# Optimization experiments

Hardware: AMD Instinct MI355X
Metric: run time of the kernel (lower is better)

The kernel has to match this reference:

```python
import jax, jax.numpy as jnp
from jax import lax
import numpy as np

B, C, H, W = 8, 1024, 32, 32
M = 32768
EPS = 1e-12  # clamp before sqrt, matching typical torch euclidean_dist


def setup_inputs() -> dict:
    key = jax.random.key(0)
    k1, k2 = jax.random.split(key)
    features = jax.random.normal(k1, (B, C, H, W), dtype=jnp.float32)
    coreset = jax.random.normal(k2, (M, C), dtype=jnp.float32)
    return {"features": features, "coreset": coreset}


def reference(features, coreset):
    # F.avg_pool2d(features, 3, 1, 1): kernel 3, stride 1, pad 1,
    # count_include_pad=True (torch default) -> window sum / 9.
    pooled = lax.reduce_window(
        features, jnp.float32(0.0), lax.add,
        window_dimensions=(1, 1, 3, 3),
        window_strides=(1, 1, 1, 1),
        padding=((0, 0), (0, 0), (1, 1), (1, 1)),
    ) / jnp.float32(9.0)
    # permute(0,2,3,1).view(B, H*W, C) then flatten batch -> [N, C]
    emb = pooled.transpose(0, 2, 3, 1).reshape(-1, C)  # [N=B*H*W, C]
    x2 = jnp.sum(emb * emb, axis=-1, keepdims=True)        # [N, 1]
    y2 = jnp.sum(coreset * coreset, axis=-1)               # [M]
    d2 = x2 + y2[None, :] - 2.0 * (emb @ coreset.T)        # [N, M]
    dist = jnp.sqrt(jnp.clip(d2, EPS))
    min_dist = jnp.min(dist, axis=1)                       # [N] 1-NN distance
    return min_dist
```

## Files before the change

### kernel.cpp

```cpp
#include <hip/hip_runtime.h>
#include <stdint.h>
#include <math.h>


#define N_TOT 8192
#define M_TOT 32768
#define EPS_ 1e-12f

typedef short bf16x8 __attribute__((ext_vector_type(8)));
typedef float f32x4 __attribute__((ext_vector_type(4)));

__device__ __forceinline__ unsigned short f2bf_rne(float f) {
    unsigned u = __float_as_uint(f);
    u += 0x7fffu + ((u >> 16) & 1u);
    return (unsigned short)(u >> 16);
}
__device__ __forceinline__ float bf2f(unsigned short h) {
    return __uint_as_float(((unsigned)h) << 16);
}

__global__ void init_kernel(unsigned* __restrict__ d2u, float* __restrict__ x2) {
    int i = blockIdx.x * blockDim.x + threadIdx.x;
    if (i < N_TOT) { d2u[i] = 0x7F800000u; x2[i] = 0.0f; }
}

__global__ __launch_bounds__(256) void pool_kernel(const float* __restrict__ feat,
                                                   unsigned short* __restrict__ emb,
                                                   float* __restrict__ x2) {
    int bid = blockIdx.x;
    int h  = bid & 31;
    int cc = (bid >> 5) & 31;
    int b  = bid >> 10;
    int tid = threadIdx.x;
    __shared__ float lds[32 * 97];

    const float* base = feat + ((size_t)(b * 1024 + cc * 32)) * 1024;
    int g0 = (h - 1) * 32;
    #pragma unroll
    for (int it = 0; it < 12; ++it) {
        int e = tid + it * 256;
        int ci = e / 96;
        int j  = e - ci * 96;
        int g  = g0 + j;
        float v = 0.0f;
        if (g >= 0 && g < 1024) v = base[(size_t)ci * 1024 + g];
        lds[ci * 97 + j] = v;
    }
    __syncthreads();

    int c  = tid & 31;
    int wb = tid >> 5;
    const float inv9 = 1.0f / 9.0f;
    #pragma unroll
    for (int i = 0; i < 4; ++i) {
        int w = wb + i * 8;
        float s = 0.0f;
        #pragma unroll
        for (int rr = 0; rr < 3; ++rr) {
            int rb = c * 97 + rr * 32 + w;
            s += lds[rb];
            if (w > 0)  s += lds[rb - 1];
            if (w < 31) s += lds[rb + 1];
        }
        float p = s * inv9;
        unsigned short bh = f2bf_rne(p);
        int n = b * 1024 + h * 32 + w;
        emb[(size_t)n * 1024 + cc * 32 + c] = bh;
        float pf = bf2f(bh);
        float sq = pf * pf;
        #pragma unroll
        for (int off = 1; off < 32; off <<= 1) sq += __shfl_xor(sq, off);
        if (c == 0) atomicAdd(&x2[n], sq);
    }
}

__global__ __launch_bounds__(256) void cs_kernel(const float* __restrict__ cs,
                                                 unsigned short* __restrict__ csb,
                                                 float* __restrict__ y2) {
    int row  = blockIdx.x * 4 + (threadIdx.x >> 6);
    int lane = threadIdx.x & 63;
    const float4* src = reinterpret_cast<const float4*>(cs + (size_t)row * 1024);
    ushort4* dst = reinterpret_cast<ushort4*>(csb + (size_t)row * 1024);
    float s = 0.0f;
    #pragma unroll
    for (int it = 0; it < 4; ++it) {
        float4 v = src[lane + it * 64];
        ushort4 o;
        o.x = f2bf_rne(v.x); o.y = f2bf_rne(v.y);
        o.z = f2bf_rne(v.z); o.w = f2bf_rne(v.w);
        dst[lane + it * 64] = o;
        float a = bf2f(o.x), b = bf2f(o.y), c = bf2f(o.z), d = bf2f(o.w);
        s += a * a + b * b + c * c + d * d;
    }
    #pragma unroll
    for (int off = 1; off < 64; off <<= 1) s += __shfl_xor(s, off);
    if (lane == 0) y2[row] = s;
}


#define STAGE(BUF, TT) do {                                                              \
    int t_ = (TT);                                                                       \
    _Pragma("unroll")                                                                    \
    for (int s_ = 0; s_ < 2; ++s_) {                                                     \
        __builtin_amdgcn_global_load_lds(                                                \
            (const __attribute__((address_space(1))) void*)(gA + (size_t)(s_ * 128 + rowq) * 1024 + t_ * 32 + ch * 8), \
            (__attribute__((address_space(3))) void*)(&lds[(BUF) * 16384 + s_ * 4096 + tid * 8]), 16, 0, 0); \
        __builtin_amdgcn_global_load_lds(                                                \
            (const __attribute__((address_space(1))) void*)(gB + (size_t)(s_ * 128 + rowq) * 1024 + t_ * 32 + ch * 8), \
            (__attribute__((address_space(3))) void*)(&lds[(BUF) * 16384 + 8192 + s_ * 4096 + tid * 8]), 16, 0, 0); \
    }                                                                                    \
} while (0)

#define READS_MFMA(BCUR) do {                                                            \
    bf16x8 af[8], bv[4];                                                                 \
    const unsigned short* pA = &lds[(BCUR) * 16384 + (wmBase + fr) * 32 + sx];           \
    const unsigned short* pB = &lds[(BCUR) * 16384 + 8192 + (wnBase + fr) * 32 + sx];    \
    _Pragma("unroll")                                                                    \
    for (int m = 0; m < 8; ++m) af[m] = *reinterpret_cast<const bf16x8*>(pA + m * 512);  \
    _Pragma("unroll")                                                                    \
    for (int n = 0; n < 4; ++n) bv[n] = *reinterpret_cast<const bf16x8*>(pB + n * 512);  \
    __builtin_amdgcn_s_setprio(1);                                                       \
    _Pragma("unroll")                                                                    \
    for (int m = 0; m < 8; ++m)                                                          \
        _Pragma("unroll")                                                                \
        for (int n = 0; n < 4; ++n)                                                      \
            acc[m][n] = __builtin_amdgcn_mfma_f32_16x16x32_bf16(af[m], bv[n], acc[m][n], 0, 0, 0); \
    __builtin_amdgcn_s_setprio(0);                                                       \
} while (0)

#define GEMM_ITER(BCUR, BSTG, TN) do {                                                   \
    asm volatile("s_waitcnt vmcnt(4)" ::: "memory");                                     \
    __builtin_amdgcn_s_barrier();                                                        \
    __builtin_amdgcn_sched_barrier(0);                                                   \
    STAGE(BSTG, TN);                                                                     \
    READS_MFMA(BCUR);                                                                    \
} while (0)

__global__ __launch_bounds__(512, 2) void gemm_min_kernel(const unsigned short* __restrict__ emb,
                                                          const unsigned short* __restrict__ csb,
                                                          const float* __restrict__ x2,
                                                          const float* __restrict__ y2,
                                                          unsigned* __restrict__ d2u) {
    __shared__ unsigned short lds[49152];

    int bid = blockIdx.x;
    int xcd   = bid & 7;
    int local = bid >> 3;
    int st    = local >> 4;
    int idx   = local & 15;
    int si = idx >> 2, sj = idx & 3;
    int emb_tile = (st & 7) * 4 + si;
    int cs_tile  = xcd * 16 + (st >> 3) * 4 + sj;
    int nb = emb_tile * 256;
    int mb = cs_tile * 256;

    int tid  = threadIdx.x;
    int lane = tid & 63;
    int wid  = tid >> 6;
    int wmBase = (wid >> 2) * 128;
    int wnBase = (wid & 3) * 64;

    int rowq = tid >> 2;
    int ch   = (tid & 3) ^ ((tid >> 3) & 3);
    const unsigned short* gA = emb + (size_t)nb * 1024;
    const unsigned short* gB = csb + (size_t)mb * 1024;

    int fr = lane & 15;
    int kq = lane >> 4;
    int sx = (kq ^ ((fr >> 1) & 3)) * 8;

    f32x4 acc[8][4];
    #pragma unroll
    for (int m = 0; m < 8; ++m)
        #pragma unroll
        for (int n = 0; n < 4; ++n) acc[m][n] = (f32x4){0.f, 0.f, 0.f, 0.f};

    STAGE(0, 0);
    STAGE(1, 1);

    #pragma unroll 1
    for (int u = 0; u < 30; u += 3) {
        GEMM_ITER(0, 2, u + 2);
        GEMM_ITER(1, 0, u + 3);
        GEMM_ITER(2, 1, u + 4);
    }
    asm volatile("s_waitcnt vmcnt(4)" ::: "memory");
    __builtin_amdgcn_s_barrier();
    __builtin_amdgcn_sched_barrier(0);
    READS_MFMA(0);
    asm volatile("s_waitcnt vmcnt(0)" ::: "memory");
    __builtin_amdgcn_s_barrier();
    __builtin_amdgcn_sched_barrier(0);
    READS_MFMA(1);

    int cc = lane & 15;
    int rq = (lane >> 4) * 4;
    float y2v[4];
    #pragma unroll
    for (int n = 0; n < 4; ++n) y2v[n] = y2[mb + wnBase + n * 16 + cc];

    #pragma unroll
    for (int m = 0; m < 8; ++m) {
        #pragma unroll
        for (int j = 0; j < 4; ++j) {
            float v = y2v[0] - 2.0f * acc[m][0][j];
            #pragma unroll
            for (int n = 1; n < 4; ++n) v = fminf(v, y2v[n] - 2.0f * acc[m][n][j]);
            int grow = nb + wmBase + m * 16 + rq + j;
            float d2 = x2[grow] + v;
            d2 = fmaxf(d2, EPS_);
            #pragma unroll
            for (int off = 1; off < 16; off <<= 1) d2 = fminf(d2, __shfl_xor(d2, off));
            if (cc == 0) atomicMin(&d2u[grow], __float_as_uint(d2));
        }
    }
}

__global__ void sqrt_kernel(const unsigned* __restrict__ d2u, float* __restrict__ out) {
    int i = blockIdx.x * blockDim.x + threadIdx.x;
    if (i < N_TOT) out[i] = sqrtf(__uint_as_float(d2u[i]));
}

extern "C" void kernel_launch(void* const* d_in, const int* in_sizes, int n_in,
                              void* d_out, int out_size, void* d_ws, size_t ws_size,
                              hipStream_t stream) {
    const float* feat = (const float*)d_in[0];
    const float* cs   = (const float*)d_in[1];
    float* out = (float*)d_out;

    char* ws = (char*)d_ws;
    unsigned short* emb = (unsigned short*)ws;
    unsigned short* csb = (unsigned short*)(ws + 16777216);
    float* x2 = (float*)(ws + 16777216 + 67108864);
    float* y2 = x2 + N_TOT;
    unsigned* d2u = (unsigned*)(y2 + M_TOT);

    init_kernel<<<N_TOT / 256, 256, 0, stream>>>(d2u, x2);
    pool_kernel<<<8192, 256, 0, stream>>>(feat, emb, x2);
    cs_kernel<<<M_TOT / 4, 256, 0, stream>>>(cs, csb, y2);
    gemm_min_kernel<<<4096, 512, 0, stream>>>(emb, csb, x2, y2, d2u);
    sqrt_kernel<<<N_TOT / 256, 256, 0, stream>>>(d2u, out);
}
```

Measured before the change: 905.9 us.

## Split each K-step into four barrier-synced phases interleaving LDS reads, staging and MFMA

Measured after the change: 891.0 us. Within noise of the previous version (-1.6%).

```diff
diff --git a/kernel.cpp b/kernel.cpp
--- a/kernel.cpp
+++ b/kernel.cpp
@@ -111,29 +111,53 @@
     }                                                                                    \
 } while (0)
 
-#define READS_MFMA(BCUR) do {                                                            \
-    bf16x8 af[8], bv[4];                                                                 \
-    const unsigned short* pA = &lds[(BCUR) * 16384 + (wmBase + fr) * 32 + sx];           \
-    const unsigned short* pB = &lds[(BCUR) * 16384 + 8192 + (wnBase + fr) * 32 + sx];    \
+#define STAGE_ONE(BSTG, TT, MTX, HALF)                                                   \
+    __builtin_amdgcn_global_load_lds(                                                    \
+        (const __attribute__((address_space(1))) void*)(((MTX) ? gB : gA) + (size_t)((HALF) * 128 + rowq) * 1024 + (TT) * 32 + ch * 8), \
+        (__attribute__((address_space(3))) void*)(&lds[(BSTG) * 16384 + (MTX) * 8192 + (HALF) * 4096 + tid * 8]), 16, 0, 0)
+
+#define PHASE_CORE(Q, A0, A1) do {                                                       \
+    __builtin_amdgcn_sched_barrier(0);                                                   \
+    __builtin_amdgcn_s_barrier();                                                        \
+    __builtin_amdgcn_sched_barrier(0);                                                   \
+    __builtin_amdgcn_s_setprio(1);                                                       \
     _Pragma("unroll")                                                                    \
-    for (int m = 0; m < 8; ++m) af[m] = *reinterpret_cast<const bf16x8*>(pA + m * 512);  \
+    for (int n = 0; n < 4; ++n) {                                                        \
+        acc[2*(Q)][n]   = __builtin_amdgcn_mfma_f32_16x16x32_bf16(A0, bv[n], acc[2*(Q)][n], 0, 0, 0);   \
+        acc[2*(Q)+1][n] = __builtin_amdgcn_mfma_f32_16x16x32_bf16(A1, bv[n], acc[2*(Q)+1][n], 0, 0, 0); \
+    }                                                                                    \
+    __builtin_amdgcn_s_setprio(0);                                                       \
+    __builtin_amdgcn_sched_barrier(0);                                                   \
+} while (0)
+
+#define ITER4(BCUR, BSTG, TT, DOSTAGE, VMN) do {                                         \
+    const unsigned short* pA = &lds[(BCUR) * 16384 + aoff];                              \
+    const unsigned short* pB = &lds[(BCUR) * 16384 + boff];                              \
+    bf16x8 bv[4];                                                                        \
     _Pragma("unroll")                                                                    \
     for (int n = 0; n < 4; ++n) bv[n] = *reinterpret_cast<const bf16x8*>(pB + n * 512);  \
-    __builtin_amdgcn_s_setprio(1);                                                       \
-    _Pragma("unroll")                                                                    \
-    for (int m = 0; m < 8; ++m)                                                          \
-        _Pragma("unroll")                                                                \
-        for (int n = 0; n < 4; ++n)                                                      \
-            acc[m][n] = __builtin_amdgcn_mfma_f32_16x16x32_bf16(af[m], bv[n], acc[m][n], 0, 0, 0); \
-    __builtin_amdgcn_s_setprio(0);                                                       \
-} while (0)
-
-#define GEMM_ITER(BCUR, BSTG, TN) do {                                                   \
-    asm volatile("s_waitcnt vmcnt(4)" ::: "memory");                                     \
-    __builtin_amdgcn_s_barrier();                                                        \
-    __builtin_amdgcn_sched_barrier(0);                                                   \
-    STAGE(BSTG, TN);                                                                     \
-    READS_MFMA(BCUR);                                                                    \
+    bf16x8 a0 = *reinterpret_cast<const bf16x8*>(pA + 0 * 512);                          \
+    bf16x8 a1 = *reinterpret_cast<const bf16x8*>(pA + 1 * 512);                          \
+    if (DOSTAGE) STAGE_ONE(BSTG, TT, 0, 0);                                              \
+    PHASE_CORE(0, a0, a1);                                                               \
+    __builtin_amdgcn_s_barrier();                                                        \
+    a0 = *reinterpret_cast<const bf16x8*>(pA + 2 * 512);                                 \
+    a1 = *reinterpret_cast<const bf16x8*>(pA + 3 * 512);                                 \
+    if (DOSTAGE) STAGE_ONE(BSTG, TT, 1, 0);                                              \
+    PHASE_CORE(1, a0, a1);                                                               \
+    __builtin_amdgcn_s_barrier();                                                        \
+    a0 = *reinterpret_cast<const bf16x8*>(pA + 4 * 512);                                 \
+    a1 = *reinterpret_cast<const bf16x8*>(pA + 5 * 512);                                 \
+    if (DOSTAGE) STAGE_ONE(BSTG, TT, 0, 1);                                              \
+    PHASE_CORE(2, a0, a1);                                                               \
+    __builtin_amdgcn_s_barrier();                                                        \
+    a0 = *reinterpret_cast<const bf16x8*>(pA + 6 * 512);                                 \
+    a1 = *reinterpret_cast<const bf16x8*>(pA + 7 * 512);                                 \
+    if (DOSTAGE) STAGE_ONE(BSTG, TT, 1, 1);                                              \
+    PHASE_CORE(3, a0, a1);                                                               \
+    if ((VMN) == 4) asm volatile("s_waitcnt vmcnt(4)" ::: "memory");                     \
+    if ((VMN) == 0) asm volatile("s_waitcnt vmcnt(0)" ::: "memory");                     \
+    __builtin_amdgcn_s_barrier();                                                        \
 } while (0)
 
 __global__ __launch_bounds__(512, 2) void gemm_min_kernel(const unsigned short* __restrict__ emb,
@@ -168,6 +192,8 @@
     int fr = lane & 15;
     int kq = lane >> 4;
     int sx = (kq ^ ((fr >> 1) & 3)) * 8;
+    int aoff = (wmBase + fr) * 32 + sx;
+    int boff = 8192 + (wnBase + fr) * 32 + sx;
 
     f32x4 acc[8][4];
     #pragma unroll
@@ -177,21 +203,17 @@
 
     STAGE(0, 0);
     STAGE(1, 1);
-
-    #pragma unroll 1
-    for (int u = 0; u < 30; u += 3) {
-        GEMM_ITER(0, 2, u + 2);
-        GEMM_ITER(1, 0, u + 3);
-        GEMM_ITER(2, 1, u + 4);
-    }
     asm volatile("s_waitcnt vmcnt(4)" ::: "memory");
     __builtin_amdgcn_s_barrier();
-    __builtin_amdgcn_sched_barrier(0);
-    READS_MFMA(0);
-    asm volatile("s_waitcnt vmcnt(0)" ::: "memory");
-    __builtin_amdgcn_s_barrier();
-    __builtin_amdgcn_sched_barrier(0);
-    READS_MFMA(1);
+
+    #pragma unroll 1
+    for (int t = 0; t < 30; t += 3) {
+        ITER4(0, 2, t + 2, true, 4);
+        ITER4(1, 0, t + 3, true, 4);
+        ITER4(2, 1, t + 4, true, 4);
+    }
+    ITER4(0, 0, 0, false, 0);
+    ITER4(1, 0, 0, false, -1);
 
     int cc = lane & 15;
     int rq = (lane >> 4) * 4;
```
